# Kernel tuning notes

Measured on AMD Instinct MI355X. Metric: run time of the kernel, lower is better.

The kernel has to match this reference:

```python
import jax, jax.numpy as jnp
import numpy as np

B, D, H = 131072, 256, 4
NUM_EXPERTS = 4


def setup_inputs() -> dict:
    key = jax.random.key(0)
    ks = jax.random.split(key, 32)
    s = 0.02
    w = lambda k, shape: (jax.random.normal(k, shape, jnp.float32) * s)
    z = lambda shape: jnp.zeros(shape, jnp.float32)
    return {
        "z_gat": jax.random.normal(ks[0], (B, D), jnp.float32),
        "z_gin": jax.random.normal(ks[1], (B, D), jnp.float32),
        # gate: Linear(2D -> 4)
        "gate_W": w(ks[2], (2 * D, NUM_EXPERTS)), "gate_b": z((NUM_EXPERTS,)),
        # expert 0: ConcatFusion  fc1(2D->D), fc2(D->D)
        "c_W1": w(ks[3], (2 * D, D)), "c_b1": z((D,)),
        "c_W2": w(ks[4], (D, D)), "c_b2": z((D,)),
        # expert 1: MulFusion fc1(D->D), fc2(D->D)
        "m_W1": w(ks[5], (D, D)), "m_b1": z((D,)),
        "m_W2": w(ks[6], (D, D)), "m_b2": z((D,)),
        # expert 2: CrossAttnFusion (MHA in/out proj + fc)
        "a_Wq": w(ks[7], (D, D)), "a_bq": z((D,)),
        "a_Wk": w(ks[8], (D, D)), "a_bk": z((D,)),
        "a_Wv": w(ks[9], (D, D)), "a_bv": z((D,)),
        "a_Wo": w(ks[10], (D, D)), "a_bo": z((D,)),
        "a_Wfc": w(ks[11], (D, D)), "a_bfc": z((D,)),
        # expert 3: WeightedSumFusion fc_alpha(2D->D), fc_out(D->D)
        "w_Wa": w(ks[12], (2 * D, D)), "w_ba": z((D,)),
        "w_Wo": w(ks[13], (D, D)), "w_bo": z((D,)),
    }


def reference(z_gat, z_gin, gate_W, gate_b,
              c_W1, c_b1, c_W2, c_b2,
              m_W1, m_b1, m_W2, m_b2,
              a_Wq, a_bq, a_Wk, a_bk, a_Wv, a_bv, a_Wo, a_bo, a_Wfc, a_bfc,
              w_Wa, w_ba, w_Wo, w_bo):
    x = jnp.concatenate([z_gat, z_gin], axis=-1)          # (B, 2D)
    gate_probs = jax.nn.softmax(x @ gate_W + gate_b, -1)  # (B, 4)
    topk_p, topk_i = jax.lax.top_k(gate_probs, 1)         # k = 1
    probs = topk_p[:, 0]
    idx = topk_i[:, 0]

    def concat_expert():
        h = jax.nn.relu(x @ c_W1 + c_b1)
        return h @ c_W2 + c_b2

    def mul_expert():
        h = jax.nn.relu((z_gat * z_gin) @ m_W1 + m_b1)
        return h @ m_W2 + m_b2

    def attn_expert():
        zs = jnp.stack([z_gat, z_gin], axis=1)            # (B, 2, D)
        hd = D // H
        q = (zs @ a_Wq + a_bq).reshape(-1, 2, H, hd)
        k = (zs @ a_Wk + a_bk).reshape(-1, 2, H, hd)
        v = (zs @ a_Wv + a_bv).reshape(-1, 2, H, hd)
        scale = 1.0 / float(np.sqrt(hd))
        sc = jnp.einsum('bqhd,bkhd->bhqk', q, k) * scale  # (B, H, 2, 2)
        a = jax.nn.softmax(sc, -1)
        o = jnp.einsum('bhqk,bkhd->bqhd', a, v).reshape(-1, 2, D)
        o = o @ a_Wo + a_bo                               # (B, 2, D)
        return o.mean(axis=1) @ a_Wfc + a_bfc

    def wsum_expert():
        alpha = jax.nn.sigmoid(x @ w_Wa + w_ba)
        h = alpha * z_gat + (1.0 - alpha) * z_gin
        return h @ w_Wo + w_bo

    expert_outs = [concat_expert(), mul_expert(), attn_expert(), wsum_expert()]

    output = jnp.zeros_like(z_gat)
    counts = []
    for e in range(NUM_EXPERTS):
        sel = idx == e                                    # disjoint masks since k=1
        cnt = sel.sum()
        # original: scalar mean of selected gate probs, weighting whole expert output
        avg = jnp.where(cnt > 0,
                        jnp.sum(probs * sel) / jnp.maximum(cnt, 1).astype(probs.dtype),
                        jnp.asarray(0.0, probs.dtype))
        output = output + jnp.where(sel[:, None], avg * expert_outs[e], 0.0)
        counts.append(cnt)

    usage = jnp.stack(counts).astype(jnp.float32) / B
    aux_loss = jnp.sum(usage ** 2) * float(NUM_EXPERTS)
    # dropout is identity in eval mode
    return output, aux_loss
```

## Files before the change

### kernel.cpp

```cpp
#include <hip/hip_runtime.h>
#include <math.h>

#define BN 131072
#define DD 256
#define NE 4

typedef unsigned short u16;
typedef __bf16 bf16x8 __attribute__((ext_vector_type(8)));
typedef float f32x4 __attribute__((ext_vector_type(4)));

__device__ __forceinline__ u16 f2bf(float f) {
  union { float f; unsigned int u; } v; v.f = f;
  unsigned int u = v.u;
  unsigned int r = (u + 0x7FFFu + ((u >> 16) & 1u)) >> 16;
  return (u16)r;
}
__device__ __forceinline__ float bf2f(u16 x) {
  union { unsigned int u; float f; } v; v.u = ((unsigned int)x) << 16; return v.f;
}

#define WS_SWZ_OFF 2097216
#define BCOMB_OFF  3670080

#define OFF_CW1  0
#define OFF_CW2  131072
#define OFF_MW1  196608
#define OFF_MW2  262144
#define OFF_AWQ  327680
#define OFF_AWK  393216
#define OFF_AWV  458752
#define OFF_WCB  524288
#define OFF_WWA  589824
#define OFF_WWO  720896
#define SWZ_TOTAL_GROUPS 98304

__global__ void k_init(int* __restrict__ listpos, double* __restrict__ psum) {
  int t = threadIdx.x;
  if (t < NE) { listpos[t] = 0; psum[t] = 0.0; }
}

__global__ __launch_bounds__(256) void k_wcomb(
    const float* __restrict__ Wo, const float* __restrict__ bo,
    const float* __restrict__ Wfc, const float* __restrict__ bfc,
    float* __restrict__ Wc, float* __restrict__ bc) {
  int n = threadIdx.x;
  int k = blockIdx.x;
  if (k < 256) {
    float acc = 0.f;
    #pragma unroll 8
    for (int j = 0; j < 256; ++j) acc += Wo[k * 256 + j] * Wfc[j * 256 + n];
    Wc[k * 256 + n] = acc;
  } else {
    float acc = bfc[n];
    #pragma unroll 8
    for (int j = 0; j < 256; ++j) acc += bo[j] * Wfc[j * 256 + n];
    bc[n] = acc;
  }
// ... 14 lines not shown
  #pragma unroll
  for (int t = 1; t < 10; ++t) if (g >= a.gbase[t]) i = t;
  int gl = g - a.gbase[i];
  int KS = a.KS[i], lks = a.lks[i];
  int l = gl & 63, t2 = gl >> 6;
  int ks = t2 & (KS - 1), ct = t2 >> lks;
  const float* src = a.src[i] + (size_t)(ks * 32 + ((l >> 4) << 3)) * 256 + ct * 16 + (l & 15);
  u16 tmp[8];
  #pragma unroll
  for (int j = 0; j < 8; ++j) tmp[j] = f2bf(src[(size_t)j * 256]);
  uint4 pk;
  pk.x = (unsigned)tmp[0] | ((unsigned)tmp[1] << 16);
  pk.y = (unsigned)tmp[2] | ((unsigned)tmp[3] << 16);
  pk.z = (unsigned)tmp[4] | ((unsigned)tmp[5] << 16);
  pk.w = (unsigned)tmp[6] | ((unsigned)tmp[7] << 16);
  *(uint4*)(dst + a.dstoff[i] + (size_t)gl * 8) = pk;
}

__global__ __launch_bounds__(256) void k_gate(
    const float* __restrict__ zg, const float* __restrict__ zn,
    const float* __restrict__ gW, const float* __restrict__ gb,
    int* __restrict__ listpos, double* __restrict__ psum,
    int* __restrict__ lists) {
  __shared__ float xs[32 * 257];
  __shared__ double gwd[512 * 4];
  __shared__ int    wcnt[4][4];
  __shared__ double wps[4][4];
  __shared__ int    wbase[4][4];
  int tid = threadIdx.x, lane = tid & 63, wave = tid >> 6;
  int rowbase = blockIdx.x * 256;
  for (int i = tid; i < 2048; i += 256) gwd[i] = (double)gW[i];
  double l0 = (double)gb[0], l1 = (double)gb[1], l2 = (double)gb[2], l3 = (double)gb[3];

  float4 pf[8];
  #pragma unroll
  for (int j = 0; j < 8; ++j) {
    int idx = tid + j * 256;
    int row = idx >> 3, off = idx & 7;
    pf[j] = *(const float4*)(zg + (size_t)(rowbase + row) * DD + off * 4);
  }

  for (int c = 0; c < 16; ++c) {
    __syncthreads();
    #pragma unroll
    for (int j = 0; j < 8; ++j) {
      int idx = tid + j * 256;
      int row = idx >> 3, off = idx & 7;
      float4 v = pf[j];
      xs[(off * 4 + 0) * 257 + row] = v.x;
      xs[(off * 4 + 1) * 257 + row] = v.y;
      xs[(off * 4 + 2) * 257 + row] = v.z;
      xs[(off * 4 + 3) * 257 + row] = v.w;
    }
    if (c < 15) {
      const float* src = (c + 1 < 8) ? zg : zn;
      int ko = ((c + 1) & 7) * 32;
      #pragma unroll
      for (int j = 0; j < 8; ++j) {
        int idx = tid + j * 256;
        int row = idx >> 3, off = idx & 7;
        pf[j] = *(const float4*)(src + (size_t)(rowbase + row) * DD + ko + off * 4);
      }
    }
    __syncthreads();
    const double* gp = gwd + (size_t)(c * 32) * 4;
    #pragma unroll
    for (int i = 0; i < 32; ++i) {
      double x = (double)xs[i * 257 + tid];
      l0 = fma(x, gp[i * 4 + 0], l0);
      l1 = fma(x, gp[i * 4 + 1], l1);
      l2 = fma(x, gp[i * 4 + 2], l2);
      l3 = fma(x, gp[i * 4 + 3], l3);
    }
  }

  int row = rowbase + tid;
  int e = 0; double lm = l0;
  if (l1 > lm) { lm = l1; e = 1; }
  if (l2 > lm) { lm = l2; e = 2; }
  if (l3 > lm) { lm = l3; e = 3; }
  double s = exp(l0 - lm) + exp(l1 - lm) + exp(l2 - lm) + exp(l3 - lm);
  double p = 1.0 / s;

  unsigned long long msk[4];
  int cnt[4];
  double pvs[4];
  #pragma unroll
  for (int ee = 0; ee < NE; ++ee) {
    bool mine = (e == ee);
    msk[ee] = __ballot(mine);
    cnt[ee] = __popcll(msk[ee]);
    double pv = mine ? p : 0.0;
    #pragma unroll
    for (int off = 32; off; off >>= 1) pv += __shfl_down(pv, off);
    pvs[ee] = pv;
  }
  if (lane == 0) {
    #pragma unroll
    for (int ee = 0; ee < NE; ++ee) { wcnt[wave][ee] = cnt[ee]; wps[wave][ee] = pvs[ee]; }
  }
  __syncthreads();
  if (tid < NE) {
    int ee = tid;
    int c0 = wcnt[0][ee], c1 = wcnt[1][ee], c2 = wcnt[2][ee], c3 = wcnt[3][ee];
    int tot = c0 + c1 + c2 + c3;
// ... 9 lines not shown
  }
  __syncthreads();
  #pragma unroll
  for (int ee = 0; ee < NE; ++ee) {
    if (e == ee) {
      int rank = __popcll(msk[ee] & ((1ull << lane) - 1ull));
      lists[(size_t)ee * BN + wbase[wave][ee] + rank] = row;
    }
  }
}

__global__ void k_finalize(const int* __restrict__ listpos,
                           const double* __restrict__ psum,
                           float* __restrict__ avg, float* __restrict__ aux_out) {
  if (threadIdx.x == 0) {
    double aux = 0.0;
    for (int ee = 0; ee < NE; ++ee) {
      int c = listpos[ee];
      avg[ee] = (c > 0) ? (float)(psum[ee] / (double)c) : 0.0f;
      double u = (double)c / (double)BN;
      aux += u * u;
    }
    *aux_out = (float)(aux * (double)NE);
  }
}

template <int KS, int RB>
__device__ __forceinline__ void mfma_gemm(const u16* __restrict__ A, int strideA,
                                          const u16* __restrict__ W,
                                          int wave, int lane, f32x4 acc[RB][4]) {
  int q = lane >> 4, m = lane & 15;
  #pragma unroll
  for (int ks = 0; ks < KS; ++ks) {
    bf16x8 a[RB];
    #pragma unroll
    for (int rb = 0; rb < RB; ++rb)
      a[rb] = *(const bf16x8*)(A + (rb * 16 + m) * strideA + ks * 32 + (q << 3));
    #pragma unroll
    for (int i = 0; i < 4; ++i) {
      int ct = wave * 4 + i;
      bf16x8 b = *(const bf16x8*)(W + (((ct * KS + ks) * 64 + lane) << 3));
      #pragma unroll
      for (int rb = 0; rb < RB; ++rb)
        acc[rb][i] = __builtin_amdgcn_mfma_f32_16x16x32_bf16(a[rb], b, acc[rb][i], 0, 0, 0);
    }
  }
}

template <int KS, int RB>
__device__ __forceinline__ void mfma_gemm_p(const u16* __restrict__ A, int strideA,
                                            const u16* __restrict__ W,
                                            int wave, int lane, f32x4 acc[RB][4]) {
  int q = lane >> 4, m = lane & 15;
  const u16* wb = W + (((size_t)(wave * 4 * KS) * 64 + lane) << 3);
  bf16x8 b0[4], b1[4];
  #pragma unroll
  for (int i = 0; i < 4; ++i)
    b0[i] = *(const bf16x8*)(wb + (((size_t)(i * KS) * 64) << 3));
  #pragma unroll 1
  for (int ks = 0; ks < KS; ks += 2) {
    #pragma unroll
    for (int i = 0; i < 4; ++i)
      b1[i] = *(const bf16x8*)(wb + (((size_t)(i * KS + ks + 1) * 64) << 3));
    bf16x8 a[RB];
    #pragma unroll
    for (int rb = 0; rb < RB; ++rb)
      a[rb] = *(const bf16x8*)(A + (rb * 16 + m) * strideA + ks * 32 + (q << 3));
    #pragma unroll
    for (int i = 0; i < 4; ++i)
      #pragma unroll
      for (int rb = 0; rb < RB; ++rb)
        acc[rb][i] = __builtin_amdgcn_mfma_f32_16x16x32_bf16(a[rb], b0[i], acc[rb][i], 0, 0, 0);
    if (ks + 2 < KS) {
      #pragma unroll
      for (int i = 0; i < 4; ++i)
        b0[i] = *(const bf16x8*)(wb + (((size_t)(i * KS + ks + 2) * 64) << 3));
    }
    #pragma unroll
    for (int rb = 0; rb < RB; ++rb)
      a[rb] = *(const bf16x8*)(A + (rb * 16 + m) * strideA + (ks + 1) * 32 + (q << 3));
    #pragma unroll
    for (int i = 0; i < 4; ++i)
      #pragma unroll
      for (int rb = 0; rb < RB; ++rb)
        acc[rb][i] = __builtin_amdgcn_mfma_f32_16x16x32_bf16(a[rb], b1[i], acc[rb][i], 0, 0, 0);
  }
}

__global__ __launch_bounds__(256) void k_concat(
    const float* __restrict__ zg, const float* __restrict__ zn,
    const u16* __restrict__ W1s, const float* __restrict__ b1,
    const u16* __restrict__ W2s, const float* __restrict__ b2,
    const int* __restrict__ listpos, const int* __restrict__ lists,
    const float* __restrict__ avgp, float* __restrict__ out) {
  __shared__ u16 X[32 * 520];
  __shared__ u16 H[32 * 264];
  __shared__ int rl[32];
  int n = listpos[0];
  const int* lst = lists + 0 * (size_t)BN;
  float scale = avgp[0];
  int tid = threadIdx.x, lane = tid & 63, wave = tid >> 6;
  int q = lane >> 4, m = lane & 15;

  for (int tile = blockIdx.x; tile * 32 < n; tile += gridDim.x) {
    int base = tile * 32;
    __syncthreads();
    if (tid < 32) rl[tid] = (base + tid < n) ? lst[base + tid] : -1;
    __syncthreads();
    #pragma unroll
    for (int j = 0; j < 16; ++j) {
      int t = tid + j * 256;
      int row = t >> 7, off = t & 127;
      int r = rl[row];
      float4 v = make_float4(0.f, 0.f, 0.f, 0.f);
      if (r >= 0)
        v = (off < 64) ? *(const float4*)(zg + (size_t)r * DD + off * 4)
                       : *(const float4*)(zn + (size_t)r * DD + (off - 64) * 4);
      ushort4 pk; pk.x = f2bf(v.x); pk.y = f2bf(v.y); pk.z = f2bf(v.z); pk.w = f2bf(v.w);
      *(ushort4*)(X + row * 520 + off * 4) = pk;
    }
    __syncthreads();
    f32x4 acc[2][4] = {};
    mfma_gemm<16, 2>(X, 520, W1s, wave, lane, acc);
    #pragma unroll
    for (int i = 0; i < 4; ++i) {
      int c = (wave * 4 + i) * 16 + m;
      float bb = b1[c];
      #pragma unroll
      for (int rb = 0; rb < 2; ++rb)
        #pragma unroll
        for (int r = 0; r < 4; ++r)
          H[(rb * 16 + q * 4 + r) * 264 + c] = f2bf(fmaxf(acc[rb][i][r] + bb, 0.f));
    }
    __syncthreads();
    f32x4 acc2[2][4] = {};
    mfma_gemm<8, 2>(H, 264, W2s, wave, lane, acc2);
    #pragma unroll
    for (int i = 0; i < 4; ++i) {
      int c = (wave * 4 + i) * 16 + m;
      float bb = b2[c];
      #pragma unroll
      for (int rb = 0; rb < 2; ++rb)
        #pragma unroll
        for (int r = 0; r < 4; ++r) {
          int row = rl[rb * 16 + q * 4 + r];
          if (row >= 0) out[(size_t)row * DD + c] = (acc2[rb][i][r] + bb) * scale;
        }
    }
  }
}

__global__ __launch_bounds__(256) void k_mul(
    const float* __restrict__ zg, const float* __restrict__ zn,
    const u16* __restrict__ W1s, const float* __restrict__ b1,
    const u16* __restrict__ W2s, const float* __restrict__ b2,
    const int* __restrict__ listpos, const int* __restrict__ lists,
    const float* __restrict__ avgp, float* __restrict__ out) {
  __shared__ u16 X[64 * 264];
  __shared__ u16 H[64 * 264];
  __shared__ int rl[64];
  int n = listpos[1];
  const int* lst = lists + 1 * (size_t)BN;
  float scale = avgp[1];
  int tid = threadIdx.x, lane = tid & 63, wave = tid >> 6;
  int q = lane >> 4, m = lane & 15;

  for (int tile = blockIdx.x; tile * 64 < n; tile += gridDim.x) {
    int base = tile * 64;
    __syncthreads();
    if (tid < 64) rl[tid] = (base + tid < n) ? lst[base + tid] : -1;
    __syncthreads();
    #pragma unroll
    for (int j = 0; j < 16; ++j) {
      int t = tid + j * 256;
      int row = t >> 6, off = t & 63;
      int r = rl[row];
      float4 v = make_float4(0.f, 0.f, 0.f, 0.f);
      if (r >= 0) {
        float4 g = *(const float4*)(zg + (size_t)r * DD + off * 4);
        float4 h = *(const float4*)(zn + (size_t)r * DD + off * 4);
        v = make_float4(g.x * h.x, g.y * h.y, g.z * h.z, g.w * h.w);
      }
      ushort4 pk; pk.x = f2bf(v.x); pk.y = f2bf(v.y); pk.z = f2bf(v.z); pk.w = f2bf(v.w);
      *(ushort4*)(X + row * 264 + off * 4) = pk;
    }
    __syncthreads();
    f32x4 acc[4][4] = {};
    mfma_gemm_p<8, 4>(X, 264, W1s, wave, lane, acc);
    #pragma unroll
    for (int i = 0; i < 4; ++i) {
      int c = (wave * 4 + i) * 16 + m;
      float bb = b1[c];
      #pragma unroll
      for (int rb = 0; rb < 4; ++rb)
        #pragma unroll
        for (int r = 0; r < 4; ++r)
          H[(rb * 16 + q * 4 + r) * 264 + c] = f2bf(fmaxf(acc[rb][i][r] + bb, 0.f));
    }
    __syncthreads();
    f32x4 acc2[4][4] = {};
    mfma_gemm_p<8, 4>(H, 264, W2s, wave, lane, acc2);
    #pragma unroll
    for (int i = 0; i < 4; ++i) {
      int c = (wave * 4 + i) * 16 + m;
      float bb = b2[c];
      #pragma unroll
      for (int rb = 0; rb < 4; ++rb)
        #pragma unroll
        for (int r = 0; r < 4; ++r) {
          int row = rl[rb * 16 + q * 4 + r];
          if (row >= 0) out[(size_t)row * DD + c] = (acc2[rb][i][r] + bb) * scale;
        }
    }
  }
}

__global__ __launch_bounds__(256) void k_wsum(
    const float* __restrict__ zg, const float* __restrict__ zn,
    const u16* __restrict__ Was, const float* __restrict__ ba,
    const u16* __restrict__ Wos, const float* __restrict__ bo,
    const int* __restrict__ listpos, const int* __restrict__ lists,
    const float* __restrict__ avgp, float* __restrict__ out) {
  __shared__ u16 X[32 * 520];
  __shared__ u16 H[32 * 264];
  __shared__ int rl[32];
  int n = listpos[3];
  const int* lst = lists + 3 * (size_t)BN;
  float scale = avgp[3];
  int tid = threadIdx.x, lane = tid & 63, wave = tid >> 6;
  int q = lane >> 4, m = lane & 15;

  for (int tile = blockIdx.x; tile * 32 < n; tile += gridDim.x) {
    int base = tile * 32;
    __syncthreads();
    if (tid < 32) rl[tid] = (base + tid < n) ? lst[base + tid] : -1;
    __syncthreads();
    #pragma unroll
    for (int j = 0; j < 16; ++j) {
      int t = tid + j * 256;
      int row = t >> 7, off = t & 127;
      int r = rl[row];
      float4 v = make_float4(0.f, 0.f, 0.f, 0.f);
      if (r >= 0)
        v = (off < 64) ? *(const float4*)(zg + (size_t)r * DD + off * 4)
                       : *(const float4*)(zn + (size_t)r * DD + (off - 64) * 4);
      ushort4 pk; pk.x = f2bf(v.x); pk.y = f2bf(v.y); pk.z = f2bf(v.z); pk.w = f2bf(v.w);
      *(ushort4*)(X + row * 520 + off * 4) = pk;
    }
    __syncthreads();
    f32x4 acc[2][4] = {};
    mfma_gemm<16, 2>(X, 520, Was, wave, lane, acc);
    #pragma unroll
    for (int i = 0; i < 4; ++i) {
      int c = (wave * 4 + i) * 16 + m;
      float bb = ba[c];
      #pragma unroll
      for (int rb = 0; rb < 2; ++rb)
        #pragma unroll
        for (int r = 0; r < 4; ++r) {
          int vr = rb * 16 + q * 4 + r;
          float al = 1.f / (1.f + __expf(-(acc[rb][i][r] + bb)));
          float xg = bf2f(X[vr * 520 + c]);
          float xn = bf2f(X[vr * 520 + 256 + c]);
          H[vr * 264 + c] = f2bf(al * xg + (1.f - al) * xn);
        }
    }
    __syncthreads();
    f32x4 acc2[2][4] = {};
    mfma_gemm<8, 2>(H, 264, Wos, wave, lane, acc2);
    #pragma unroll
    for (int i = 0; i < 4; ++i) {
      int c = (wave * 4 + i) * 16 + m;
      float bb = bo[c];
      #pragma unroll
      for (int rb = 0; rb < 2; ++rb)
        #pragma unroll
        for (int r = 0; r < 4; ++r) {
          int row = rl[rb * 16 + q * 4 + r];
          if (row >= 0) out[(size_t)row * DD + c] = (acc2[rb][i][r] + bb) * scale;
        }
    }
  }
}

__global__ __launch_bounds__(256) void k_attn(
    const float* __restrict__ zg, const float* __restrict__ zn,
    const u16* __restrict__ Wqs, const float* __restrict__ bq,
    const u16* __restrict__ Wks, const float* __restrict__ bk,
    const u16* __restrict__ Wvs, const float* __restrict__ bv,
    const int* __restrict__ listpos, const int* __restrict__ lists,
    float* __restrict__ out) {
  __shared__ u16 X[64 * 264];
  __shared__ int rl[32];
  int n = listpos[2];
  const int* lst = lists + 2 * (size_t)BN;
  int tid = threadIdx.x, lane = tid & 63, wave = tid >> 6;
  int q = lane >> 4, m = lane & 15;

  float bqv[4], bkv[4], bvv[4];
  #pragma unroll
  for (int i = 0; i < 4; ++i) {
    int c = wave * 64 + i * 16 + m;
    bqv[i] = bq[c]; bkv[i] = bk[c]; bvv[i] = bv[c];
  }

  for (int tile = blockIdx.x; tile * 32 < n; tile += gridDim.x) {
    int base = tile * 32;
    __syncthreads();
    if (tid < 32) rl[tid] = (base + tid < n) ? lst[base + tid] : -1;
    __syncthreads();
    #pragma unroll
    for (int j = 0; j < 16; ++j) {
      int t = tid + j * 256;
      int v = t >> 6, off = t & 63;
      int r = rl[v >> 1];
      float4 val = make_float4(0.f, 0.f, 0.f, 0.f);
      if (r >= 0)
        val = (v & 1) ? *(const float4*)(zn + (size_t)r * DD + off * 4)
                      : *(const float4*)(zg + (size_t)r * DD + off * 4);
      ushort4 pk; pk.x = f2bf(val.x); pk.y = f2bf(val.y); pk.z = f2bf(val.z); pk.w = f2bf(val.w);
      *(ushort4*)(X + v * 264 + off * 4) = pk;
    }
    __syncthreads();
    f32x4 qa[4][4] = {};
    mfma_gemm_p<8, 4>(X, 264, Wqs, wave, lane, qa);
    #pragma unroll
    for (int rb = 0; rb < 4; ++rb)
      #pragma unroll
      for (int i = 0; i < 4; ++i)
        #pragma unroll
        for (int r = 0; r < 4; ++r) qa[rb][i][r] += bqv[i];
    f32x4 ka[4][4] = {};
    mfma_gemm_p<8, 4>(X, 264, Wks, wave, lane, ka);
    #pragma unroll
    for (int rb = 0; rb < 4; ++rb)
      #pragma unroll
      for (int i = 0; i < 4; ++i)
        #pragma unroll
        for (int r = 0; r < 4; ++r) ka[rb][i][r] += bkv[i];
    float C0[4][2], C1[4][2];
    #pragma unroll
    for (int rb = 0; rb < 4; ++rb) {
      #pragma unroll
      for (int pr = 0; pr < 2; ++pr) {
        float p00 = 0.f, p01 = 0.f, p10 = 0.f, p11 = 0.f;
        #pragma unroll
        for (int i = 0; i < 4; ++i) {
          float q0 = qa[rb][i][2 * pr], q1 = qa[rb][i][2 * pr + 1];
          float ke = ka[rb][i][2 * pr], ko = ka[rb][i][2 * pr + 1];
          p00 += q0 * ke; p01 += q0 * ko;
          p10 += q1 * ke; p11 += q1 * ko;
        }
        #pragma unroll
        for (int msk = 1; msk < 16; msk <<= 1) {
          p00 += __shfl_xor(p00, msk);
          p01 += __shfl_xor(p01, msk);
          p10 += __shfl_xor(p10, msk);
          p11 += __shfl_xor(p11, msk);
        }
        float s00 = 1.f / (1.f + __expf((p01 - p00) * 0.125f));
        float s10 = 1.f / (1.f + __expf((p11 - p10) * 0.125f));
        float c0 = 0.5f * (s00 + s10);
        C0[rb][pr] = c0; C1[rb][pr] = 1.f - c0;
      }
    }
    f32x4 va[4][4] = {};
    mfma_gemm_p<8, 4>(X, 264, Wvs, wave, lane, va);
    #pragma unroll
    for (int rb = 0; rb < 4; ++rb)
      #pragma unroll
      for (int pr = 0; pr < 2; ++pr) {
        int rloc = rb * 8 + q * 2 + pr;
        int grow = rl[rloc];
        if (grow >= 0) {
          #pragma unroll
          for (int i = 0; i < 4; ++i) {
            float mv = C0[rb][pr] * va[rb][i][2 * pr]
                     + C1[rb][pr] * va[rb][i][2 * pr + 1] + bvv[i];
            out[(size_t)grow * DD + wave * 64 + i * 16 + m] = mv;
          }
        }
      }
  }
}

__global__ __launch_bounds__(256) void k_attn_fc(
    const u16* __restrict__ Wcs, const float* __restrict__ bc,
    const int* __restrict__ listpos, const int* __restrict__ lists,
    const float* __restrict__ avgp, float* __restrict__ out) {
  __shared__ u16 Mb[32 * 264];
  __shared__ int rl[32];
  int n = listpos[2];
  const int* lst = lists + 2 * (size_t)BN;
  float scale = avgp[2];
  int tid = threadIdx.x, lane = tid & 63, wave = tid >> 6;
  int q = lane >> 4, m = lane & 15;

  for (int tile = blockIdx.x; tile * 32 < n; tile += gridDim.x) {
    int base = tile * 32;
    __syncthreads();
    if (tid < 32) rl[tid] = (base + tid < n) ? lst[base + tid] : -1;
    __syncthreads();
    #pragma unroll
    for (int j = 0; j < 8; ++j) {
      int t = tid + j * 256;
      int row = t >> 6, off = t & 63;
      int r = rl[row];
      float4 v = make_float4(0.f, 0.f, 0.f, 0.f);
      if (r >= 0) v = *(const float4*)(out + (size_t)r * DD + off * 4);
      ushort4 pk; pk.x = f2bf(v.x); pk.y = f2bf(v.y); pk.z = f2bf(v.z); pk.w = f2bf(v.w);
      *(ushort4*)(Mb + row * 264 + off * 4) = pk;
    }
    __syncthreads();
    f32x4 acc[2][4] = {};
    mfma_gemm<8, 2>(Mb, 264, Wcs, wave, lane, acc);
    #pragma unroll
    for (int i = 0; i < 4; ++i) {
      int c = (wave * 4 + i) * 16 + m;
      float bb = bc[c];
      #pragma unroll
      for (int rb = 0; rb < 2; ++rb)
        #pragma unroll
        for (int r = 0; r < 4; ++r) {
          int row = rl[rb * 16 + q * 4 + r];
          if (row >= 0) out[(size_t)row * DD + c] = (acc[rb][i][r] + bb) * scale;
        }
    }
  }
}

extern "C" void kernel_launch(void* const* d_in, const int* in_sizes, int n_in,
                              void* d_out, int out_size, void* d_ws, size_t ws_size,
                              hipStream_t stream) {
  const float* zg   = (const float*)d_in[0];
  const float* zn   = (const float*)d_in[1];
  const float* gW   = (const float*)d_in[2];
  const float* gb   = (const float*)d_in[3];
  const float* cW1  = (const float*)d_in[4];
  const float* cb1  = (const float*)d_in[5];
  const float* cW2  = (const float*)d_in[6];
  const float* cb2  = (const float*)d_in[7];
  const float* mW1  = (const float*)d_in[8];
  const float* mb1  = (const float*)d_in[9];
  const float* mW2  = (const float*)d_in[10];
  const float* mb2  = (const float*)d_in[11];
  const float* aWq  = (const float*)d_in[12];
  const float* abq  = (const float*)d_in[13];
  const float* aWk  = (const float*)d_in[14];
  const float* abk  = (const float*)d_in[15];
// ... 13 lines not shown
  double* psum  = (double*)ws;
  int* listpos  = (int*)(ws + 32);
  float* avg    = (float*)(ws + 48);
  int* lists    = (int*)(ws + 64);
  u16* wsw      = (u16*)(ws + WS_SWZ_OFF);
  float* wcf32  = (float*)(ws + 64);
  float* bcomb  = (float*)(ws + BCOMB_OFF);

  SwzArgs sa;
  const float* srcs[10] = {cW1, cW2, mW1, mW2, aWq, aWk, aWv, wcf32, wWa, wWo};
  const int   kss[10]  = {16, 8, 8, 8, 8, 8, 8, 8, 16, 8};
  const int   offs[10] = {OFF_CW1, OFF_CW2, OFF_MW1, OFF_MW2, OFF_AWQ, OFF_AWK,
                          OFF_AWV, OFF_WCB, OFF_WWA, OFF_WWO};
  int gb_acc = 0;
  for (int i = 0; i < 10; ++i) {
    sa.src[i] = srcs[i];
    sa.KS[i] = kss[i];
    sa.lks[i] = (kss[i] == 16) ? 4 : 3;
    sa.dstoff[i] = offs[i];
    sa.gbase[i] = gb_acc;
    gb_acc += kss[i] * 1024;
  }

  hipLaunchKernelGGL(k_init, dim3(1), dim3(64), 0, stream, listpos, psum);
  hipLaunchKernelGGL(k_wcomb, dim3(257), dim3(256), 0, stream,
                     aWo, abo, aWfc, abfc, wcf32, bcomb);
  hipLaunchKernelGGL(k_swz, dim3(SWZ_TOTAL_GROUPS / 256), dim3(256), 0, stream, sa, wsw);
  hipLaunchKernelGGL(k_gate, dim3(BN / 256), dim3(256), 0, stream,
                     zg, zn, gW, gb, listpos, psum, lists);
  hipLaunchKernelGGL(k_finalize, dim3(1), dim3(64), 0, stream,
                     listpos, psum, avg, out + (size_t)BN * DD);
  hipLaunchKernelGGL(k_concat, dim3(1024), dim3(256), 0, stream,
                     zg, zn, wsw + OFF_CW1, cb1, wsw + OFF_CW2, cb2, listpos, lists, avg, out);
  hipLaunchKernelGGL(k_mul, dim3(512), dim3(256), 0, stream,
                     zg, zn, wsw + OFF_MW1, mb1, wsw + OFF_MW2, mb2, listpos, lists, avg, out);
  hipLaunchKernelGGL(k_attn, dim3(1024), dim3(256), 0, stream,
                     zg, zn, wsw + OFF_AWQ, abq, wsw + OFF_AWK, abk, wsw + OFF_AWV, abv,
                     listpos, lists, out);
  hipLaunchKernelGGL(k_attn_fc, dim3(1024), dim3(256), 0, stream,
                     wsw + OFF_WCB, bcomb, listpos, lists, avg, out);
  hipLaunchKernelGGL(k_wsum, dim3(1024), dim3(256), 0, stream,
                     zg, zn, wsw + OFF_WWA, wba, wsw + OFF_WWO, wbo, listpos, lists, avg, out);
}
```

Measured before the change: 711.9 us.

## Fuse expert kernels into one launch and split gate K-reduction across threads

Merges the five per-expert kernels (concat, mul, attention, attention-fc, wsum) into a single k_experts launch that partitions its grid into fixed block ranges per expert, so experts run concurrently instead of serially. The attention path now processes 16-row tiles and appears to fold the output projection into the same kernel instead of a separate pass. The gate kernel halves rows per block and splits the K reduction across two thread halves, combined through shared memory, to increase parallelism. The combined kernel takes the largest shared-memory footprint of any branch, which may reduce occupancy, and the fixed per-expert block split can leave some blocks idle when expert counts are imbalanced.

```diff
diff --git a/kernel.cpp b/kernel.cpp
--- a/kernel.cpp
+++ b/kernel.cpp
@@ -33,6 +33,12 @@
 #define OFF_WWA  589824
 #define OFF_WWO  720896
 #define SWZ_TOTAL_GROUPS 98304
+
+#define G_ATTN   768
+#define G_CONCAT 768
+#define G_MUL    768
+#define G_WSUM   768
+#define G_TOTAL  3072
 
 __global__ void k_init(int* __restrict__ listpos, double* __restrict__ psum) {
   int t = threadIdx.x;
@@ -93,19 +99,23 @@
     const float* __restrict__ gW, const float* __restrict__ gb,
     int* __restrict__ listpos, double* __restrict__ psum,
     int* __restrict__ lists) {
-  __shared__ float xs[32 * 257];
+  __shared__ float xs[32 * 129];
   __shared__ double gwd[512 * 4];
+  __shared__ double xr[128 * 4];
   __shared__ int    wcnt[4][4];
   __shared__ double wps[4][4];
   __shared__ int    wbase[4][4];
   int tid = threadIdx.x, lane = tid & 63, wave = tid >> 6;
-  int rowbase = blockIdx.x * 256;
+  int rlocal = tid & 127, khalf = tid >> 7;
+  int rowbase = blockIdx.x * 128;
   for (int i = tid; i < 2048; i += 256) gwd[i] = (double)gW[i];
-  double l0 = (double)gb[0], l1 = (double)gb[1], l2 = (double)gb[2], l3 = (double)gb[3];
-
-  float4 pf[8];
+  double l0, l1, l2, l3;
+  if (khalf) { l0 = l1 = l2 = l3 = 0.0; }
+  else { l0 = (double)gb[0]; l1 = (double)gb[1]; l2 = (double)gb[2]; l3 = (double)gb[3]; }
+
+  float4 pf[4];
   #pragma unroll
-  for (int j = 0; j < 8; ++j) {
+  for (int j = 0; j < 4; ++j) {
     int idx = tid + j * 256;
     int row = idx >> 3, off = idx & 7;
     pf[j] = *(const float4*)(zg + (size_t)(rowbase + row) * DD + off * 4);
@@ -114,30 +124,31 @@
   for (int c = 0; c < 16; ++c) {
     __syncthreads();
     #pragma unroll
-    for (int j = 0; j < 8; ++j) {
+    for (int j = 0; j < 4; ++j) {
       int idx = tid + j * 256;
       int row = idx >> 3, off = idx & 7;
       float4 v = pf[j];
-      xs[(off * 4 + 0) * 257 + row] = v.x;
-      xs[(off * 4 + 1) * 257 + row] = v.y;
-      xs[(off * 4 + 2) * 257 + row] = v.z;
-      xs[(off * 4 + 3) * 257 + row] = v.w;
+      xs[(off * 4 + 0) * 129 + row] = v.x;
+      xs[(off * 4 + 1) * 129 + row] = v.y;
+      xs[(off * 4 + 2) * 129 + row] = v.z;
+      xs[(off * 4 + 3) * 129 + row] = v.w;
     }
     if (c < 15) {
       const float* src = (c + 1 < 8) ? zg : zn;
       int ko = ((c + 1) & 7) * 32;
       #pragma unroll
-      for (int j = 0; j < 8; ++j) {
+      for (int j = 0; j < 4; ++j) {
         int idx = tid + j * 256;
         int row = idx >> 3, off = idx & 7;
         pf[j] = *(const float4*)(src + (size_t)(rowbase + row) * DD + ko + off * 4);
       }
     }
     __syncthreads();
-    const double* gp = gwd + (size_t)(c * 32) * 4;
-    #pragma unroll
-    for (int i = 0; i < 32; ++i) {
-      double x = (double)xs[i * 257 + tid];
+    const double* gp = gwd + (size_t)(c * 32 + khalf * 16) * 4;
+    int xbase = (khalf * 16) * 129 + rlocal;
+    #pragma unroll
+    for (int i = 0; i < 16; ++i) {
+      double x = (double)xs[xbase + i * 129];
       l0 = fma(x, gp[i * 4 + 0], l0);
       l1 = fma(x, gp[i * 4 + 1], l1);
       l2 = fma(x, gp[i * 4 + 2], l2);
@@ -145,13 +156,25 @@
     }
   }
 
-  int row = rowbase + tid;
-  int e = 0; double lm = l0;
-  if (l1 > lm) { lm = l1; e = 1; }
-  if (l2 > lm) { lm = l2; e = 2; }
-  if (l3 > lm) { lm = l3; e = 3; }
-  double s = exp(l0 - lm) + exp(l1 - lm) + exp(l2 - lm) + exp(l3 - lm);
-  double p = 1.0 / s;
+  __syncthreads();
+  if (khalf) {
+    xr[rlocal * 4 + 0] = l0; xr[rlocal * 4 + 1] = l1;
+    xr[rlocal * 4 + 2] = l2; xr[rlocal * 4 + 3] = l3;
+  }
+  __syncthreads();
+  int e = -1;
+  double p = 0.0;
+  if (!khalf) {
+    l0 += xr[rlocal * 4 + 0]; l1 += xr[rlocal * 4 + 1];
+    l2 += xr[rlocal * 4 + 2]; l3 += xr[rlocal * 4 + 3];
+    e = 0; double lm = l0;
+    if (l1 > lm) { lm = l1; e = 1; }
+    if (l2 > lm) { lm = l2; e = 2; }
+    if (l3 > lm) { lm = l3; e = 3; }
+    double s = exp(l0 - lm) + exp(l1 - lm) + exp(l2 - lm) + exp(l3 - lm);
+    p = 1.0 / s;
+  }
+  int row = rowbase + rlocal;
 
   unsigned long long msk[4];
   int cnt[4];
@@ -207,28 +230,6 @@
       aux += u * u;
     }
     *aux_out = (float)(aux * (double)NE);
-  }
-}
-
-template <int KS, int RB>
-__device__ __forceinline__ void mfma_gemm(const u16* __restrict__ A, int strideA,
-                                          const u16* __restrict__ W,
-                                          int wave, int lane, f32x4 acc[RB][4]) {
-  int q = lane >> 4, m = lane & 15;
-  #pragma unroll
-  for (int ks = 0; ks < KS; ++ks) {
-    bf16x8 a[RB];
-    #pragma unroll
-    for (int rb = 0; rb < RB; ++rb)
-      a[rb] = *(const bf16x8*)(A + (rb * 16 + m) * strideA + ks * 32 + (q << 3));
-    #pragma unroll
-    for (int i = 0; i < 4; ++i) {
-      int ct = wave * 4 + i;
-      bf16x8 b = *(const bf16x8*)(W + (((ct * KS + ks) * 64 + lane) << 3));
-      #pragma unroll
-      for (int rb = 0; rb < RB; ++rb)
-        acc[rb][i] = __builtin_amdgcn_mfma_f32_16x16x32_bf16(a[rb], b, acc[rb][i], 0, 0, 0);
-    }
   }
 }
 
@@ -272,344 +273,291 @@
   }
 }
 
-__global__ __launch_bounds__(256) void k_concat(
-    const float* __restrict__ zg, const float* __restrict__ zn,
-    const u16* __restrict__ W1s, const float* __restrict__ b1,
-    const u16* __restrict__ W2s, const float* __restrict__ b2,
-    const int* __restrict__ listpos, const int* __restrict__ lists,
-    const float* __restrict__ avgp, float* __restrict__ out) {
-  __shared__ u16 X[32 * 520];
-  __shared__ u16 H[32 * 264];
+struct ExpArgs {
+  const float* zg; const float* zn;
+  const u16* CW1; const u16* CW2; const float* cb1; const float* cb2;
+  const u16* MW1; const u16* MW2; const float* mb1; const float* mb2;
+  const u16* AWQ; const u16* AWK; const u16* AWV;
+  const float* abq; const float* abk; const float* abv;
+  const u16* WCB; const float* bcomb;
+  const u16* WWA; const u16* WWO; const float* wba; const float* wbo;
+  const int* listpos; const int* lists; const float* avgp;
+  float* out;
+};
+
+__global__ __launch_bounds__(256) void k_experts(ExpArgs A) {
+  __shared__ __align__(16) u16 smem[25088];
   __shared__ int rl[32];
-  int n = listpos[0];
-  const int* lst = lists + 0 * (size_t)BN;
-  float scale = avgp[0];
   int tid = threadIdx.x, lane = tid & 63, wave = tid >> 6;
   int q = lane >> 4, m = lane & 15;
-
-  for (int tile = blockIdx.x; tile * 32 < n; tile += gridDim.x) {
-    int base = tile * 32;
-    __syncthreads();
-    if (tid < 32) rl[tid] = (base + tid < n) ? lst[base + tid] : -1;
-    __syncthreads();
-    #pragma unroll
-    for (int j = 0; j < 16; ++j) {
-      int t = tid + j * 256;
-      int row = t >> 7, off = t & 127;
-      int r = rl[row];
-      float4 v = make_float4(0.f, 0.f, 0.f, 0.f);
-      if (r >= 0)
-        v = (off < 64) ? *(const float4*)(zg + (size_t)r * DD + off * 4)
-                       : *(const float4*)(zn + (size_t)r * DD + (off - 64) * 4);
-      ushort4 pk; pk.x = f2bf(v.x); pk.y = f2bf(v.y); pk.z = f2bf(v.z); pk.w = f2bf(v.w);
-      *(ushort4*)(X + row * 520 + off * 4) = pk;
-    }
-    __syncthreads();
-    f32x4 acc[2][4] = {};
-    mfma_gemm<16, 2>(X, 520, W1s, wave, lane, acc);
+  int bid = blockIdx.x;
+
+  if (bid < G_ATTN) {
+    int bidl = bid;
+    int n = A.listpos[2];
+    const int* lst = A.lists + 2 * (size_t)BN;
+    float scale = A.avgp[2];
+    u16* X  = smem;
+    u16* Mb = smem + 8448;
+    float bqv[4], bkv[4], bvv[4];
     #pragma unroll
     for (int i = 0; i < 4; ++i) {
-      int c = (wave * 4 + i) * 16 + m;
-      float bb = b1[c];
+      int c = wave * 64 + i * 16 + m;
+      bqv[i] = A.abq[c]; bkv[i] = A.abk[c]; bvv[i] = A.abv[c];
+    }
+    for (int tile = bidl; tile * 16 < n; tile += G_ATTN) {
+      int base = tile * 16;
+      __syncthreads();
+      if (tid < 16) rl[tid] = (base + tid < n) ? lst[base + tid] : -1;
+      __syncthreads();
+      #pragma unroll
+      for (int j = 0; j < 8; ++j) {
+        int t = tid + j * 256;
+        int v = t >> 6, off = t & 63;
+        int r = rl[v >> 1];
+        float4 val = make_float4(0.f, 0.f, 0.f, 0.f);
+        if (r >= 0)
+          val = (v & 1) ? *(const float4*)(A.zn + (size_t)r * DD + off * 4)
+                        : *(const float4*)(A.zg + (size_t)r * DD + off * 4);
+        ushort4 pk; pk.x = f2bf(val.x); pk.y = f2bf(val.y); pk.z = f2bf(val.z); pk.w = f2bf(val.w);
+        *(ushort4*)(X + v * 264 + off * 4) = pk;
+      }
+      __syncthreads();
+      f32x4 qa[2][4] = {};
+      mfma_gemm_p<8, 2>(X, 264, A.AWQ, wave, lane, qa);
       #pragma unroll
       for (int rb = 0; rb < 2; ++rb)
         #pragma unroll
-        for (int r = 0; r < 4; ++r)
-          H[(rb * 16 + q * 4 + r) * 264 + c] = f2bf(fmaxf(acc[rb][i][r] + bb, 0.f));
-    }
-    __syncthreads();
-    f32x4 acc2[2][4] = {};
-    mfma_gemm<8, 2>(H, 264, W2s, wave, lane, acc2);
-    #pragma unroll
-    for (int i = 0; i < 4; ++i) {
-      int c = (wave * 4 + i) * 16 + m;
-      float bb = b2[c];
+        for (int i = 0; i < 4; ++i)
+          #pragma unroll
+          for (int r = 0; r < 4; ++r) qa[rb][i][r] += bqv[i];
+      f32x4 ka[2][4] = {};
+      mfma_gemm_p<8, 2>(X, 264, A.AWK, wave, lane, ka);
       #pragma unroll
       for (int rb = 0; rb < 2; ++rb)
         #pragma unroll
-        for (int r = 0; r < 4; ++r) {
-          int row = rl[rb * 16 + q * 4 + r];
-          if (row >= 0) out[(size_t)row * DD + c] = (acc2[rb][i][r] + bb) * scale;
+        for (int i = 0; i < 4; ++i)
+          #pragma unroll
+          for (int r = 0; r < 4; ++r) ka[rb][i][r] += bkv[i];
+      float C0[2][2], C1[2][2];
+      #pragma unroll
+      for (int rb = 0; rb < 2; ++rb) {
+        #pragma unroll
+        for (int pr = 0; pr < 2; ++pr) {
+          float p00 = 0.f, p01 = 0.f, p10 = 0.f, p11 = 0.f;
+          #pragma unroll
+          for (int i = 0; i < 4; ++i) {
+            float q0 = qa[rb][i][2 * pr], q1 = qa[rb][i][2 * pr + 1];
+            float ke = ka[rb][i][2 * pr], ko = ka[rb][i][2 * pr + 1];
+            p00 += q0 * ke; p01 += q0 * ko;
+            p10 += q1 * ke; p11 += q1 * ko;
+          }
+          #pragma unroll
+          for (int msk = 1; msk < 16; msk <<= 1) {
+            p00 += __shfl_xor(p00, msk);
+            p01 += __shfl_xor(p01, msk);
+            p10 += __shfl_xor(p10, msk);
+            p11 += __shfl_xor(p11, msk);
+          }
+          float s00 = 1.f / (1.f + __expf((p01 - p00) * 0.125f));
+          float s10 = 1.f / (1.f + __expf((p11 - p10) * 0.125f));
+          float c0 = 0.5f * (s00 + s10);
+          C0[rb][pr] = c0; C1[rb][pr] = 1.f - c0;
         }
-    }
-  }
-}
-
-__global__ __launch_bounds__(256) void k_mul(
-    const float* __restrict__ zg, const float* __restrict__ zn,
-    const u16* __restrict__ W1s, const float* __restrict__ b1,
-    const u16* __restrict__ W2s, const float* __restrict__ b2,
-    const int* __restrict__ listpos, const int* __restrict__ lists,
-    const float* __restrict__ avgp, float* __restrict__ out) {
-  __shared__ u16 X[64 * 264];
-  __shared__ u16 H[64 * 264];
-  __shared__ int rl[64];
-  int n = listpos[1];
-  const int* lst = lists + 1 * (size_t)BN;
-  float scale = avgp[1];
-  int tid = threadIdx.x, lane = tid & 63, wave = tid >> 6;
-  int q = lane >> 4, m = lane & 15;
-
-  for (int tile = blockIdx.x; tile * 64 < n; tile += gridDim.x) {
-    int base = tile * 64;
-    __syncthreads();
-    if (tid < 64) rl[tid] = (base + tid < n) ? lst[base + tid] : -1;
-    __syncthreads();
-    #pragma unroll
-    for (int j = 0; j < 16; ++j) {
-      int t = tid + j * 256;
-      int row = t >> 6, off = t & 63;
-      int r = rl[row];
-      float4 v = make_float4(0.f, 0.f, 0.f, 0.f);
-      if (r >= 0) {
-        float4 g = *(const float4*)(zg + (size_t)r * DD + off * 4);
-        float4 h = *(const float4*)(zn + (size_t)r * DD + off * 4);
-        v = make_float4(g.x * h.x, g.y * h.y, g.z * h.z, g.w * h.w);
-      }
-      ushort4 pk; pk.x = f2bf(v.x); pk.y = f2bf(v.y); pk.z = f2bf(v.z); pk.w = f2bf(v.w);
-      *(ushort4*)(X + row * 264 + off * 4) = pk;
-    }
-    __syncthreads();
-    f32x4 acc[4][4] = {};
-    mfma_gemm_p<8, 4>(X, 264, W1s, wave, lane, acc);
-    #pragma unroll
-    for (int i = 0; i < 4; ++i) {
-      int c = (wave * 4 + i) * 16 + m;
-      float bb = b1[c];
-      #pragma unroll
-      for (int rb = 0; rb < 4; ++rb)
-        #pragma unroll
-        for (int r = 0; r < 4; ++r)
-          H[(rb * 16 + q * 4 + r) * 264 + c] = f2bf(fmaxf(acc[rb][i][r] + bb, 0.f));
-    }
-    __syncthreads();
-    f32x4 acc2[4][4] = {};
-    mfma_gemm_p<8, 4>(H, 264, W2s, wave, lane, acc2);
-    #pragma unroll
-    for (int i = 0; i < 4; ++i) {
-      int c = (wave * 4 + i) * 16 + m;
-      float bb = b2[c];
-      #pragma unroll
-      for (int rb = 0; rb < 4; ++rb)
-        #pragma unroll
-        for (int r = 0; r < 4; ++r) {
-          int row = rl[rb * 16 + q * 4 + r];
-          if (row >= 0) out[(size_t)row * DD + c] = (acc2[rb][i][r] + bb) * scale;
-        }
-    }
-  }
-}
-
-__global__ __launch_bounds__(256) void k_wsum(
-    const float* __restrict__ zg, const float* __restrict__ zn,
-    const u16* __restrict__ Was, const float* __restrict__ ba,
-    const u16* __restrict__ Wos, const float* __restrict__ bo,
-    const int* __restrict__ listpos, const int* __restrict__ lists,
-    const float* __restrict__ avgp, float* __restrict__ out) {
-  __shared__ u16 X[32 * 520];
-  __shared__ u16 H[32 * 264];
-  __shared__ int rl[32];
-  int n = listpos[3];
-  const int* lst = lists + 3 * (size_t)BN;
-  float scale = avgp[3];
-  int tid = threadIdx.x, lane = tid & 63, wave = tid >> 6;
-  int q = lane >> 4, m = lane & 15;
-
-  for (int tile = blockIdx.x; tile * 32 < n; tile += gridDim.x) {
-    int base = tile * 32;
-    __syncthreads();
-    if (tid < 32) rl[tid] = (base + tid < n) ? lst[base + tid] : -1;
-    __syncthreads();
-    #pragma unroll
-    for (int j = 0; j < 16; ++j) {
-      int t = tid + j * 256;
-      int row = t >> 7, off = t & 127;
-      int r = rl[row];
-      float4 v = make_float4(0.f, 0.f, 0.f, 0.f);
-      if (r >= 0)
-        v = (off < 64) ? *(const float4*)(zg + (size_t)r * DD + off * 4)
-                       : *(const float4*)(zn + (size_t)r * DD + (off - 64) * 4);
-      ushort4 pk; pk.x = f2bf(v.x); pk.y = f2bf(v.y); pk.z = f2bf(v.z); pk.w = f2bf(v.w);
-      *(ushort4*)(X + row * 520 + off * 4) = pk;
-    }
-    __syncthreads();
-    f32x4 acc[2][4] = {};
-    mfma_gemm<16, 2>(X, 520, Was, wave, lane, acc);
-    #pragma unroll
-    for (int i = 0; i < 4; ++i) {
-      int c = (wave * 4 + i) * 16 + m;
-      float bb = ba[c];
+      }
+      f32x4 va[2][4] = {};
+      mfma_gemm_p<8, 2>(X, 264, A.AWV, wave, lane, va);
       #pragma unroll
       for (int rb = 0; rb < 2; ++rb)
         #pragma unroll
-        for (int r = 0; r < 4; ++r) {
-          int vr = rb * 16 + q * 4 + r;
-          float al = 1.f / (1.f + __expf(-(acc[rb][i][r] + bb)));
-          float xg = bf2f(X[vr * 520 + c]);
-          float xn = bf2f(X[vr * 520 + 256 + c]);
-          H[vr * 264 + c] = f2bf(al * xg + (1.f - al) * xn);
-        }
-    }
-    __syncthreads();
-    f32x4 acc2[2][4] = {};
-    mfma_gemm<8, 2>(H, 264, Wos, wave, lane, acc2);
-    #pragma unroll
-    for (int i = 0; i < 4; ++i) {
-      int c = (wave * 4 + i) * 16 + m;
-      float bb = bo[c];
-      #pragma unroll
-      for (int rb = 0; rb < 2; ++rb)
-        #pragma unroll
-        for (int r = 0; r < 4; ++r) {
-          int row = rl[rb * 16 + q * 4 + r];
-          if (row >= 0) out[(size_t)row * DD + c] = (acc2[rb][i][r] + bb) * scale;
-        }
-    }
-  }
-}
-
-__global__ __launch_bounds__(256) void k_attn(
-    const float* __restrict__ zg, const float* __restrict__ zn,
-    const u16* __restrict__ Wqs, const float* __restrict__ bq,
-    const u16* __restrict__ Wks, const float* __restrict__ bk,
-    const u16* __restrict__ Wvs, const float* __restrict__ bv,
-    const int* __restrict__ listpos, const int* __restrict__ lists,
-    float* __restrict__ out) {
-  __shared__ u16 X[64 * 264];
-  __shared__ int rl[32];
-  int n = listpos[2];
-  const int* lst = lists + 2 * (size_t)BN;
-  int tid = threadIdx.x, lane = tid & 63, wave = tid >> 6;
-  int q = lane >> 4, m = lane & 15;
-
-  float bqv[4], bkv[4], bvv[4];
-  #pragma unroll
-  for (int i = 0; i < 4; ++i) {
-    int c = wave * 64 + i * 16 + m;
-    bqv[i] = bq[c]; bkv[i] = bk[c]; bvv[i] = bv[c];
-  }
-
-  for (int tile = blockIdx.x; tile * 32 < n; tile += gridDim.x) {
-    int base = tile * 32;
-    __syncthreads();
-    if (tid < 32) rl[tid] = (base + tid < n) ? lst[base + tid] : -1;
-    __syncthreads();
-    #pragma unroll
-    for (int j = 0; j < 16; ++j) {
-      int t = tid + j * 256;
-      int v = t >> 6, off = t & 63;
-      int r = rl[v >> 1];
-      float4 val = make_float4(0.f, 0.f, 0.f, 0.f);
-      if (r >= 0)
-        val = (v & 1) ? *(const float4*)(zn + (size_t)r * DD + off * 4)
-                      : *(const float4*)(zg + (size_t)r * DD + off * 4);
-      ushort4 pk; pk.x = f2bf(val.x); pk.y = f2bf(val.y); pk.z = f2bf(val.z); pk.w = f2bf(val.w);
-      *(ushort4*)(X + v * 264 + off * 4) = pk;
-    }
-    __syncthreads();
-    f32x4 qa[4][4] = {};
-    mfma_gemm_p<8, 4>(X, 264, Wqs, wave, lane, qa);
-    #pragma unroll
-    for (int rb = 0; rb < 4; ++rb)
-      #pragma unroll
-      for (int i = 0; i < 4; ++i)
-        #pragma unroll
-        for (int r = 0; r < 4; ++r) qa[rb][i][r] += bqv[i];
-    f32x4 ka[4][4] = {};
-    mfma_gemm_p<8, 4>(X, 264, Wks, wave, lane, ka);
-    #pragma unroll
-    for (int rb = 0; rb < 4; ++rb)
-      #pragma unroll
-      for (int i = 0; i < 4; ++i)
-        #pragma unroll
-        for (int r = 0; r < 4; ++r) ka[rb][i][r] += bkv[i];
-    float C0[4][2], C1[4][2];
-    #pragma unroll
-    for (int rb = 0; rb < 4; ++rb) {
-      #pragma unroll
-      for (int pr = 0; pr < 2; ++pr) {
-        float p00 = 0.f, p01 = 0.f, p10 = 0.f, p11 = 0.f;
-        #pragma unroll
-        for (int i = 0; i < 4; ++i) {
-          float q0 = qa[rb][i][2 * pr], q1 = qa[rb][i][2 * pr + 1];
-          float ke = ka[rb][i][2 * pr], ko = ka[rb][i][2 * pr + 1];
-          p00 += q0 * ke; p01 += q0 * ko;
-          p10 += q1 * ke; p11 += q1 * ko;
-        }
-        #pragma unroll
-        for (int msk = 1; msk < 16; msk <<= 1) {
-          p00 += __shfl_xor(p00, msk);
-          p01 += __shfl_xor(p01, msk);
-          p10 += __shfl_xor(p10, msk);
-          p11 += __shfl_xor(p11, msk);
-        }
-        float s00 = 1.f / (1.f + __expf((p01 - p00) * 0.125f));
-        float s10 = 1.f / (1.f + __expf((p11 - p10) * 0.125f));
-        float c0 = 0.5f * (s00 + s10);
-        C0[rb][pr] = c0; C1[rb][pr] = 1.f - c0;
-      }
-    }
-    f32x4 va[4][4] = {};
-    mfma_gemm_p<8, 4>(X, 264, Wvs, wave, lane, va);
-    #pragma unroll
-    for (int rb = 0; rb < 4; ++rb)
-      #pragma unroll
-      for (int pr = 0; pr < 2; ++pr) {
-        int rloc = rb * 8 + q * 2 + pr;
-        int grow = rl[rloc];
-        if (grow >= 0) {
+        for (int pr = 0; pr < 2; ++pr) {
+          int rloc = rb * 8 + q * 2 + pr;
           #pragma unroll
           for (int i = 0; i < 4; ++i) {
             float mv = C0[rb][pr] * va[rb][i][2 * pr]
                      + C1[rb][pr] * va[rb][i][2 * pr + 1] + bvv[i];
-            out[(size_t)grow * DD + wave * 64 + i * 16 + m] = mv;
+            Mb[rloc * 264 + wave * 64 + i * 16 + m] = f2bf(mv);
           }
         }
-      }
-  }
-}
-
-__global__ __launch_bounds__(256) void k_attn_fc(
-    const u16* __restrict__ Wcs, const float* __restrict__ bc,
-    const int* __restrict__ listpos, const int* __restrict__ lists,
-    const float* __restrict__ avgp, float* __restrict__ out) {
-  __shared__ u16 Mb[32 * 264];
-  __shared__ int rl[32];
-  int n = listpos[2];
-  const int* lst = lists + 2 * (size_t)BN;
-  float scale = avgp[2];
-  int tid = threadIdx.x, lane = tid & 63, wave = tid >> 6;
-  int q = lane >> 4, m = lane & 15;
-
-  for (int tile = blockIdx.x; tile * 32 < n; tile += gridDim.x) {
-    int base = tile * 32;
-    __syncthreads();
-    if (tid < 32) rl[tid] = (base + tid < n) ? lst[base + tid] : -1;
-    __syncthreads();
-    #pragma unroll
-    for (int j = 0; j < 8; ++j) {
-      int t = tid + j * 256;
-      int row = t >> 6, off = t & 63;
-      int r = rl[row];
-      float4 v = make_float4(0.f, 0.f, 0.f, 0.f);
-      if (r >= 0) v = *(const float4*)(out + (size_t)r * DD + off * 4);
-      ushort4 pk; pk.x = f2bf(v.x); pk.y = f2bf(v.y); pk.z = f2bf(v.z); pk.w = f2bf(v.w);
-      *(ushort4*)(Mb + row * 264 + off * 4) = pk;
-    }
-    __syncthreads();
-    f32x4 acc[2][4] = {};
-    mfma_gemm<8, 2>(Mb, 264, Wcs, wave, lane, acc);
-    #pragma unroll
-    for (int i = 0; i < 4; ++i) {
-      int c = (wave * 4 + i) * 16 + m;
-      float bb = bc[c];
-      #pragma unroll
-      for (int rb = 0; rb < 2; ++rb)
+      __syncthreads();
+      f32x4 ac[1][4] = {};
+      mfma_gemm_p<8, 1>(Mb, 264, A.WCB, wave, lane, ac);
+      #pragma unroll
+      for (int i = 0; i < 4; ++i) {
+        int c = (wave * 4 + i) * 16 + m;
+        float bb = A.bcomb[c];
         #pragma unroll
         for (int r = 0; r < 4; ++r) {
-          int row = rl[rb * 16 + q * 4 + r];
-          if (row >= 0) out[(size_t)row * DD + c] = (acc[rb][i][r] + bb) * scale;
+          int row = rl[q * 4 + r];
+          if (row >= 0) A.out[(size_t)row * DD + c] = (ac[0][i][r] + bb) * scale;
         }
+      }
+    }
+  } else if (bid < G_ATTN + G_CONCAT) {
+    int bidl = bid - G_ATTN;
+    int n = A.listpos[0];
+    const int* lst = A.lists + 0 * (size_t)BN;
+    float scale = A.avgp[0];
+    u16* X = smem;
+    u16* H = smem + 16640;
+    for (int tile = bidl; tile * 32 < n; tile += G_CONCAT) {
+      int base = tile * 32;
+      __syncthreads();
+      if (tid < 32) rl[tid] = (base + tid < n) ? lst[base + tid] : -1;
+      __syncthreads();
+      #pragma unroll
+      for (int j = 0; j < 16; ++j) {
+        int t = tid + j * 256;
+        int row = t >> 7, off = t & 127;
+        int r = rl[row];
+        float4 v = make_float4(0.f, 0.f, 0.f, 0.f);
+        if (r >= 0)
+          v = (off < 64) ? *(const float4*)(A.zg + (size_t)r * DD + off * 4)
+                         : *(const float4*)(A.zn + (size_t)r * DD + (off - 64) * 4);
+        ushort4 pk; pk.x = f2bf(v.x); pk.y = f2bf(v.y); pk.z = f2bf(v.z); pk.w = f2bf(v.w);
+        *(ushort4*)(X + row * 520 + off * 4) = pk;
+      }
+      __syncthreads();
+      f32x4 acc[2][4] = {};
+      mfma_gemm_p<16, 2>(X, 520, A.CW1, wave, lane, acc);
+      #pragma unroll
+      for (int i = 0; i < 4; ++i) {
+        int c = (wave * 4 + i) * 16 + m;
+        float bb = A.cb1[c];
+        #pragma unroll
+        for (int rb = 0; rb < 2; ++rb)
+          #pragma unroll
+          for (int r = 0; r < 4; ++r)
+            H[(rb * 16 + q * 4 + r) * 264 + c] = f2bf(fmaxf(acc[rb][i][r] + bb, 0.f));
+      }
+      __syncthreads();
+      f32x4 acc2[2][4] = {};
+      mfma_gemm_p<8, 2>(H, 264, A.CW2, wave, lane, acc2);
+      #pragma unroll
+      for (int i = 0; i < 4; ++i) {
+        int c = (wave * 4 + i) * 16 + m;
+        float bb = A.cb2[c];
+        #pragma unroll
+        for (int rb = 0; rb < 2; ++rb)
+          #pragma unroll
+          for (int r = 0; r < 4; ++r) {
+            int row = rl[rb * 16 + q * 4 + r];
+            if (row >= 0) A.out[(size_t)row * DD + c] = (acc2[rb][i][r] + bb) * scale;
+          }
+      }
+    }
+  } else if (bid < G_ATTN + G_CONCAT + G_MUL) {
+    int bidl = bid - (G_ATTN + G_CONCAT);
+    int n = A.listpos[1];
+    const int* lst = A.lists + 1 * (size_t)BN;
+    float scale = A.avgp[1];
+    u16* X = smem;
+    u16* H = smem + 8448;
+    for (int tile = bidl; tile * 32 < n; tile += G_MUL) {
+      int base = tile * 32;
+      __syncthreads();
+      if (tid < 32) rl[tid] = (base + tid < n) ? lst[base + tid] : -1;
+      __syncthreads();
+      #pragma unroll
+      for (int j = 0; j < 8; ++j) {
+        int t = tid + j * 256;
+        int row = t >> 6, off = t & 63;
+        int r = rl[row];
+        float4 v = make_float4(0.f, 0.f, 0.f, 0.f);
+        if (r >= 0) {
+          float4 g = *(const float4*)(A.zg + (size_t)r * DD + off * 4);
+          float4 h = *(const float4*)(A.zn + (size_t)r * DD + off * 4);
+          v = make_float4(g.x * h.x, g.y * h.y, g.z * h.z, g.w * h.w);
+        }
+        ushort4 pk; pk.x = f2bf(v.x); pk.y = f2bf(v.y); pk.z = f2bf(v.z); pk.w = f2bf(v.w);
+        *(ushort4*)(X + row * 264 + off * 4) = pk;
+      }
+      __syncthreads();
+      f32x4 acc[2][4] = {};
+      mfma_gemm_p<8, 2>(X, 264, A.MW1, wave, lane, acc);
+      #pragma unroll
+      for (int i = 0; i < 4; ++i) {
+        int c = (wave * 4 + i) * 16 + m;
+        float bb = A.mb1[c];
+        #pragma unroll
+        for (int rb = 0; rb < 2; ++rb)
+          #pragma unroll
+          for (int r = 0; r < 4; ++r)
+            H[(rb * 16 + q * 4 + r) * 264 + c] = f2bf(fmaxf(acc[rb][i][r] + bb, 0.f));
+      }
+      __syncthreads();
+      f32x4 acc2[2][4] = {};
+      mfma_gemm_p<8, 2>(H, 264, A.MW2, wave, lane, acc2);
+      #pragma unroll
+      for (int i = 0; i < 4; ++i) {
+        int c = (wave * 4 + i) * 16 + m;
+        float bb = A.mb2[c];
+        #pragma unroll
+        for (int rb = 0; rb < 2; ++rb)
+          #pragma unroll
+          for (int r = 0; r < 4; ++r) {
+            int row = rl[rb * 16 + q * 4 + r];
+            if (row >= 0) A.out[(size_t)row * DD + c] = (acc2[rb][i][r] + bb) * scale;
+          }
+      }
+    }
+  } else {
+    int bidl = bid - (G_ATTN + G_CONCAT + G_MUL);
+    int n = A.listpos[3];
+    const int* lst = A.lists + 3 * (size_t)BN;
+    float scale = A.avgp[3];
+    u16* X = smem;
+    u16* H = smem + 16640;
+    for (int tile = bidl; tile * 32 < n; tile += G_WSUM) {
+      int base = tile * 32;
+      __syncthreads();
+      if (tid < 32) rl[tid] = (base + tid < n) ? lst[base + tid] : -1;
+      __syncthreads();
+      #pragma unroll
+      for (int j = 0; j < 16; ++j) {
+        int t = tid + j * 256;
+        int row = t >> 7, off = t & 127;
+        int r = rl[row];
+        float4 v = make_float4(0.f, 0.f, 0.f, 0.f);
+        if (r >= 0)
+          v = (off < 64) ? *(const float4*)(A.zg + (size_t)r * DD + off * 4)
+                         : *(const float4*)(A.zn + (size_t)r * DD + (off - 64) * 4);
+        ushort4 pk; pk.x = f2bf(v.x); pk.y = f2bf(v.y); pk.z = f2bf(v.z); pk.w = f2bf(v.w);
+        *(ushort4*)(X + row * 520 + off * 4) = pk;
+      }
+      __syncthreads();
+      f32x4 acc[2][4] = {};
+      mfma_gemm_p<16, 2>(X, 520, A.WWA, wave, lane, acc);
+      #pragma unroll
+      for (int i = 0; i < 4; ++i) {
+        int c = (wave * 4 + i) * 16 + m;
+        float bb = A.wba[c];
+        #pragma unroll
+        for (int rb = 0; rb < 2; ++rb)
+          #pragma unroll
+          for (int r = 0; r < 4; ++r) {
+            int vr = rb * 16 + q * 4 + r;
+            float al = 1.f / (1.f + __expf(-(acc[rb][i][r] + bb)));
+            float xg = bf2f(X[vr * 520 + c]);
+            float xn = bf2f(X[vr * 520 + 256 + c]);
+            H[vr * 264 + c] = f2bf(al * xg + (1.f - al) * xn);
+          }
+      }
+      __syncthreads();
+      f32x4 acc2[2][4] = {};
+      mfma_gemm_p<8, 2>(H, 264, A.WWO, wave, lane, acc2);
+      #pragma unroll
+      for (int i = 0; i < 4; ++i) {
+        int c = (wave * 4 + i) * 16 + m;
+        float bb = A.wbo[c];
+        #pragma unroll
+        for (int rb = 0; rb < 2; ++rb)
+          #pragma unroll
+          for (int r = 0; r < 4; ++r) {
+            int row = rl[rb * 16 + q * 4 + r];
+            if (row >= 0) A.out[(size_t)row * DD + c] = (acc2[rb][i][r] + bb) * scale;
+          }
+      }
     }
   }
 }
@@ -669,23 +617,24 @@
     gb_acc += kss[i] * 1024;
   }
 
+  ExpArgs ea;
+  ea.zg = zg; ea.zn = zn;
+  ea.CW1 = wsw + OFF_CW1; ea.CW2 = wsw + OFF_CW2; ea.cb1 = cb1; ea.cb2 = cb2;
+  ea.MW1 = wsw + OFF_MW1; ea.MW2 = wsw + OFF_MW2; ea.mb1 = mb1; ea.mb2 = mb2;
+  ea.AWQ = wsw + OFF_AWQ; ea.AWK = wsw + OFF_AWK; ea.AWV = wsw + OFF_AWV;
+  ea.abq = abq; ea.abk = abk; ea.abv = abv;
+  ea.WCB = wsw + OFF_WCB; ea.bcomb = bcomb;
+  ea.WWA = wsw + OFF_WWA; ea.WWO = wsw + OFF_WWO; ea.wba = wba; ea.wbo = wbo;
+  ea.listpos = listpos; ea.lists = lists; ea.avgp = avg;
+  ea.out = out;
+
   hipLaunchKernelGGL(k_init, dim3(1), dim3(64), 0, stream, listpos, psum);
   hipLaunchKernelGGL(k_wcomb, dim3(257), dim3(256), 0, stream,
                      aWo, abo, aWfc, abfc, wcf32, bcomb);
   hipLaunchKernelGGL(k_swz, dim3(SWZ_TOTAL_GROUPS / 256), dim3(256), 0, stream, sa, wsw);
-  hipLaunchKernelGGL(k_gate, dim3(BN / 256), dim3(256), 0, stream,
+  hipLaunchKernelGGL(k_gate, dim3(BN / 128), dim3(256), 0, stream,
                      zg, zn, gW, gb, listpos, psum, lists);
   hipLaunchKernelGGL(k_finalize, dim3(1), dim3(64), 0, stream,
                      listpos, psum, avg, out + (size_t)BN * DD);
-  hipLaunchKernelGGL(k_concat, dim3(1024), dim3(256), 0, stream,
-                     zg, zn, wsw + OFF_CW1, cb1, wsw + OFF_CW2, cb2, listpos, lists, avg, out);
-  hipLaunchKernelGGL(k_mul, dim3(512), dim3(256), 0, stream,
-                     zg, zn, wsw + OFF_MW1, mb1, wsw + OFF_MW2, mb2, listpos, lists, avg, out);
-  hipLaunchKernelGGL(k_attn, dim3(1024), dim3(256), 0, stream,
-                     zg, zn, wsw + OFF_AWQ, abq, wsw + OFF_AWK, abk, wsw + OFF_AWV, abv,
-                     listpos, lists, out);
-  hipLaunchKernelGGL(k_attn_fc, dim3(1024), dim3(256), 0, stream,
-                     wsw + OFF_WCB, bcomb, listpos, lists, avg, out);
-  hipLaunchKernelGGL(k_wsum, dim3(1024), dim3(256), 0, stream,
-                     zg, zn, wsw + OFF_WWA, wba, wsw + OFF_WWO, wbo, listpos, lists, avg, out);
-}
+  hipLaunchKernelGGL(k_experts, dim3(G_TOTAL), dim3(256), 0, stream, ea);
+}
```

New measurement: 614.3 us. -13.7%, faster.
